# Kernel tuning notes

Hardware: AMD Instinct MI355X
Metric: run time of the kernel (lower is better)

Reference implementation:

```python
import jax, jax.numpy as jnp
import numpy as np

HID = 128          # args.hidden_dim
B = 8              # batch_size
N = 256            # num_nodes per graph (uniform)
L = 48             # num_colours / levels per graph (uniform, logk=False)
CELLS = B * N * L  # 98304 'cell' nodes
E = 250000         # edges per edge type
STEPS = 2          # args.msg_passing_steps


def setup_inputs() -> dict:
    key = jax.random.key(0)
    ks = jax.random.split(key, 20)
    s = 0.05
    d = {}
    d["q"] = jax.random.randint(ks[0], (CELLS,), 0, 3)
    d["edge_src"] = jax.random.randint(ks[1], (2, E), 0, CELLS)
    d["edge_dst"] = jax.random.randint(ks[2], (2, E), 0, CELLS)
    d["embed"] = jax.random.normal(ks[3], (3, HID), jnp.float32) * s
    # per-edge-type 4-layer MLP (stacked along axis 0: [intra, inter])
    d["msg_W0"] = jax.random.normal(ks[4], (2, HID, 2 * HID), jnp.float32) * s
    d["msg_b0"] = jnp.zeros((2, HID), jnp.float32)
    d["msg_W1"] = jax.random.normal(ks[5], (2, HID, HID), jnp.float32) * s
    d["msg_b1"] = jnp.zeros((2, HID), jnp.float32)
    d["msg_W2"] = jax.random.normal(ks[6], (2, HID, HID), jnp.float32) * s
    d["msg_b2"] = jnp.zeros((2, HID), jnp.float32)
    d["msg_W3"] = jax.random.normal(ks[7], (2, HID, HID), jnp.float32) * s
    d["msg_b3"] = jnp.zeros((2, HID), jnp.float32)
    # LSTMCell, bias=False: input = cat(x, m_intra, m_inter) -> 3*HID
    d["lstm_Wih"] = jax.random.normal(ks[8], (4 * HID, 3 * HID), jnp.float32) * s
    d["lstm_Whh"] = jax.random.normal(ks[9], (4 * HID, HID), jnp.float32) * s
    d["score_w"] = jax.random.normal(ks[10], (1, HID), jnp.float32) * s
    return d


def reference(q, edge_src, edge_dst, embed, msg_W0, msg_b0, msg_W1, msg_b1,
              msg_W2, msg_b2, msg_W3, msg_b3, lstm_Wih, lstm_Whh, score_w):
    x = embed[q]  # [CELLS, HID]

    def edge_msgs(h):
        msgs = []
        for et in range(2):  # structural loop over the 2 edge types
            src, dst = edge_src[et], edge_dst[et]
            m = jnp.concatenate([h[src], h[dst]], axis=-1)  # [E, 2H]
            m = jax.nn.relu(m @ msg_W0[et].T + msg_b0[et])
            m = jax.nn.relu(m @ msg_W1[et].T + msg_b1[et])
            m = jax.nn.relu(m @ msg_W2[et].T + msg_b2[et])
            m = m @ msg_W3[et].T + msg_b3[et]
            msgs.append(jax.ops.segment_sum(m, dst, num_segments=CELLS))
        return msgs

    def step(carry, _):
        h, rh, rc = carry
        m_intra, m_inter = edge_msgs(h)
        lstm_in = jnp.concatenate([x, m_intra, m_inter], axis=-1)  # [CELLS, 3H]
        gates = lstm_in @ lstm_Wih.T + rh @ lstm_Whh.T              # [CELLS, 4H]
        i, f, g, o = jnp.split(gates, 4, axis=-1)
        nc = jax.nn.sigmoid(f) * rc + jax.nn.sigmoid(i) * jnp.tanh(g)
        nh = jax.nn.sigmoid(o) * jnp.tanh(nc)
        return (nh, nh, nc), nh

    zeros = jnp.zeros_like(x)
    _, outs = jax.lax.scan(step, (x, zeros, zeros), None, length=STEPS)
    # outs: [STEPS, CELLS, HID]; uniform sizes make get_padded_tensor a reshape:
    # [STEPS, B, L, N, HID] -> score -> view(STEPS, B*N*L)
    logits = (outs @ score_w[0]).reshape(STEPS, B * L * N)
    return logits
```

## Files before the change

### kernel.cpp

```cpp
#include <hip/hip_runtime.h>

#define HID 128
#define CELLS 98304
#define NE 250000
#define NSTEPS 2
#define NWIN 3912

typedef __attribute__((ext_vector_type(8))) short short8;
typedef __attribute__((ext_vector_type(4))) float f32x4;
typedef __attribute__((ext_vector_type(4))) unsigned int u32x4;
typedef unsigned short u16;

__device__ __forceinline__ int permf(int s) { return ((s & 7) << 4) | (s >> 3); }
__device__ __forceinline__ int nat_of_pos(int p) {
  int l = p & 63, hf = p >> 6;
  int slot = ((l >> 2) << 3) + (hf << 2) + (l & 3);
  return ((slot & 7) << 4) | (slot >> 3);
}

__device__ __forceinline__ u16 f2bf(float f) {
  unsigned int u = __builtin_bit_cast(unsigned int, f);
  u += 0x7fffu + ((u >> 16) & 1u);
  return (u16)(u >> 16);
}
__device__ __forceinline__ float bf2f(u16 s) {
  unsigned int u = ((unsigned int)s) << 16;
  return __builtin_bit_cast(float, u);
}
__device__ __forceinline__ unsigned int cvtpk_bf16(float lo, float hi) {
  unsigned int r;
  asm("v_cvt_pk_bf16_f32 %0, %1, %2" : "=v"(r) : "v"(lo), "v"(hi));
  return r;
}
__device__ __forceinline__ float sigm(float x) { return 1.f / (1.f + __expf(-x)); }
__device__ __forceinline__ float tanha(float x) { return 1.f - 2.f / (__expf(2.f * x) + 1.f); }

__device__ __forceinline__ void gload_lds16(const u16* g, u16* l) {
  __builtin_amdgcn_global_load_lds(
      (const __attribute__((address_space(1))) unsigned int*)(const void*)g,
      (__attribute__((address_space(3))) unsigned int*)(void*)l, 16, 0, 0);
}

__device__ __forceinline__ void stage_w(const u16* __restrict__ ws, u16* wl, int w, int lane) {
  #pragma unroll
  for (int i = 0; i < 2; ++i)
    gload_lds16(ws + i * 4096 + w * 512 + lane * 8, wl + i * 4096 + w * 512);
}

__global__ void prep_kernel(
    const float* __restrict__ W0, const float* __restrict__ W1,
    const float* __restrict__ W2, const float* __restrict__ W3,
    const float* __restrict__ b0, const float* __restrict__ b1,
    const float* __restrict__ b2, const float* __restrict__ b3,
    const float* __restrict__ Wih, const float* __restrict__ Whh,
    const float* __restrict__ embed, const float* __restrict__ sw,
    u16* __restrict__ W0b, u16* __restrict__ W123b,
    u16* __restrict__ Wcb, float* __restrict__ bp,
    u16* __restrict__ embp, float* __restrict__ swp)
{
  int idx = blockIdx.x * 256 + threadIdx.x;
  if (idx < 65536) {
    int et = idx >> 15, t = (idx >> 13) & 3, n = (idx >> 6) & 127, s = idx & 63;
    int g = s >> 3, j = s & 7;
    int gn = g ^ (n & 7);
    W0b[idx] = f2bf(W0[(et * 128 + n) * 256 + t * 64 + gn * 8 + j]);
    return;
  }
  idx -= 65536;
  if (idx < 98304) {
    int which = idx >> 15, r = idx & 32767;
    int et = r >> 14, hh = (r >> 13) & 1, n = (r >> 6) & 127, s = r & 63;
    int g = s >> 3, j = s & 7;
    int gn = g ^ (n & 7);
    const float* W = which == 0 ? W1 : (which == 1 ? W2 : W3);
    W123b[which * 32768 + r] = f2bf(W[(et * 128 + n) * 128 + permf(hh * 64 + gn * 8 + j)]);
    return;
  }
  idx -= 98304;
  if (idx < 262144) {
    int kc = idx >> 15, r = idx & 32767;
    int n = r >> 6, s = r & 63;
    int gp = s >> 3, j = s & 7;
    int k = kc * 64 + ((gp ^ (n & 7)) << 3) + j;
    int blk = k >> 7, s7 = k & 127;
    int k7 = (blk == 1 || blk == 2) ? nat_of_pos(s7) : s7;
    float v = (blk < 3) ? Wih[n * 384 + blk * 128 + k7] : Whh[n * 128 + k7];
    Wcb[idx] = f2bf(v);
    return;
  }
  idx -= 262144;
  if (idx < 1024) {
    int l = idx >> 8, r = idx & 255;
    int et = r >> 7, s = r & 127;
    const float* b = l == 0 ? b0 : (l == 1 ? b1 : (l == 2 ? b2 : b3));
    bp[idx] = b[et * 128 + permf(s)];
    return;
  }
  idx -= 1024;
  if (idx < 384) {
    embp[idx] = f2bf(embed[idx]);
    return;
  }
  idx -= 384;
  if (idx < 128) swp[idx] = sw[idx];
}

__global__ void init_kernel(const int* __restrict__ q, const u16* __restrict__ embp,
                            u16* __restrict__ xb, u16* __restrict__ h)
{
  int idx = blockIdx.x * 256 + threadIdx.x;
  int c = idx >> 7, s = idx & 127;
  u16 v = embp[q[c] * 128 + s];
  xb[idx] = v;
  h[idx] = v;
}

__global__ void hist_kernel(const int* __restrict__ edst, int* __restrict__ counts)
{
  int idx = blockIdx.x * 256 + threadIdx.x;
  if (idx >= 2 * NE) return;
  int et = (idx >= NE) ? 1 : 0;
  atomicAdd(&counts[et * CELLS + edst[idx]], 1);
}

__global__ void scan1_kernel(const int* __restrict__ counts, int* __restrict__ S,
                             int* __restrict__ btot)
{
  __shared__ int sh[1024];
  const int t = threadIdx.x, b = blockIdx.x;
  const int i = b * 1024 + t;
  int v = counts[i];
  sh[t] = v;
  __syncthreads();
  int acc = v;
  for (int off = 1; off < 1024; off <<= 1) {
    int add = (t >= off) ? sh[t - off] : 0;
    __syncthreads();
    acc += add;
    sh[t] = acc;
    __syncthreads();
  }
  S[i] = acc - v;
  if (t == 1023) btot[b] = acc;
}

__global__ void scan2_kernel(const int* __restrict__ btot, int* __restrict__ boffs,
                             int* __restrict__ S)
{
  __shared__ int sh[256];
  const int t = threadIdx.x;
  int v = (t < 192) ? btot[t] : 0;
  sh[t] = v;
  __syncthreads();
  int acc = v;
  for (int off = 1; off < 256; off <<= 1) {
    int add = (t >= off) ? sh[t - off] : 0;
    __syncthreads();
    acc += add;
    sh[t] = acc;
    __syncthreads();
  }
  if (t < 192) boffs[t] = acc - v;
  if (t == 0) S[2 * CELLS] = 2 * NE;
}

__global__ void scan3_kernel(int* __restrict__ S, const int* __restrict__ boffs)
{
  const int i = blockIdx.x * 1024 + threadIdx.x;
  S[i] += boffs[blockIdx.x];
}

__global__ void scatter_kernel(const int* __restrict__ esrc, const int* __restrict__ edst,
                               const int* __restrict__ S, int* __restrict__ fill,
                               int* __restrict__ ssrc, int* __restrict__ sdst)
{
  int idx = blockIdx.x * 256 + threadIdx.x;
  if (idx >= 2 * NE) return;
  int et = (idx >= NE) ? 1 : 0;
  int d = edst[idx];
  int pos = atomicAdd(&fill[et * CELLS + d], 1);
  int slot = S[et * CELLS + d] - et * NE + pos;
  sdst[et * NE + slot] = d;
  ssrc[et * NE + slot] = esrc[idx];
}

__device__ __forceinline__ void bias_relu_store(f32x4 (&acc)[4][8], const float* __restrict__ bl,
                                                u16* __restrict__ ab, int q, int c)
{
  float bias[8];
  #pragma unroll
  for (int j = 0; j < 8; ++j) bias[j] = bl[c * 8 + j];
  #pragma unroll
  for (int mt = 0; mt < 4; ++mt) {
    #pragma unroll
    for (int r = 0; r < 4; ++r) {
      const int rowl = mt * 16 + 4 * q + r;
      u32x4 t;
      #pragma unroll
      for (int p = 0; p < 4; ++p) {
        float v0 = acc[mt][2 * p][r] + bias[2 * p];
        float v1 = acc[mt][2 * p + 1][r] + bias[2 * p + 1];
        v0 = v0 > 0.f ? v0 : 0.f;
        v1 = v1 > 0.f ? v1 : 0.f;
        t[p] = cvtpk_bf16(v0, v1);
      }
      *(u32x4*)(ab + rowl * 128 + ((c ^ (rowl & 15)) << 3)) = t;
    }
  }
}

__launch_bounds__(512, 2)
__global__ void msg_kernel(
    const u16* __restrict__ h,
    const int* __restrict__ ssrc, const int* __restrict__ sdst,
    const int* __restrict__ S,
    const u16* __restrict__ W0b, const u16* __restrict__ W123b,
    const float* __restrict__ bp,
    u16* __restrict__ m0, u16* __restrict__ m1,
    int* __restrict__ side_dst, float* __restrict__ side_part)
{
  __shared__ u16 abuf[8][64 * 128];
  __shared__ u16 wbuf[2][128 * 64];
  const int et = blockIdx.y;
  const int tid = threadIdx.x;
  const int w = tid >> 6, lane = tid & 63, q = lane >> 4, c = lane & 15;
  const int ebase = blockIdx.x * 512 + w * 64;
  const int win = blockIdx.x * 8 + w;
  const int* __restrict__ src = ssrc + et * NE;
  const int* __restrict__ dst = sdst + et * NE;
  u16* __restrict__ msgs = (et == 0) ? m0 : m1;
  u16* ab = abuf[w];

  int eS = ebase + lane;
  if (eS >= NE) eS = NE - 1;
  const int srow = src[eS];

  int rowD[4];
  #pragma unroll
  for (int mt = 0; mt < 4; ++mt) {
    int e = ebase + mt * 16 + c;
    if (e >= NE) e = NE - 1;
    rowD[mt] = dst[e];
  }

  #pragma unroll
  for (int i = 0; i < 16; ++i) {
    const int r = i * 4 + (lane >> 4);
    const int grow = __shfl(srow, r);
    const int cg = lane & 15;
    gload_lds16(h + (size_t)grow * 128 + ((cg ^ (r & 15)) << 3), ab + i * 512);
  }
  stage_w(W0b + (et * 4 + 2) * 8192, wbuf[0], w, lane);

  const int eL = ebase + lane;
  const int dval = (eL < NE) ? dst[eL] : -1;
  int rpS = 0, rpE = 0;
  if (dval >= 0) {
    rpS = S[et * CELLS + dval] - et * NE;
    rpE = S[et * CELLS + dval + 1] - et * NE;
  }
  const int dlagged = __shfl_up(dval, 1);
  const bool headp = (lane == 0) | (dval != dlagged);
  const unsigned long long tails = (__ballot(headp) >> 1) | (1ull << 63);
  const unsigned long long intmask = __ballot(dval >= 0 && rpS >= ebase && rpE <= ebase + 64);

  const f32x4 zf = {0.f, 0.f, 0.f, 0.f};
  f32x4 acc[4][8];
  #pragma unroll
  for (int mt = 0; mt < 4; ++mt)
    #pragma unroll
    for (int nt = 0; nt < 8; ++nt) acc[mt][nt] = zf;

  asm volatile("s_waitcnt vmcnt(0)" ::: "memory");
  __syncthreads();

  #pragma unroll 1
  for (int i = 0; i < 10; ++i) {
    if (i < 9) {
      const int j = i + 1;
      const u16* wsrc;
      if (j < 4) {
        const int t = (j < 2) ? (j + 2) : (j - 2);
        wsrc = W0b + (et * 4 + t) * 8192;
      } else {
        const int li = j - 4;
        wsrc = W123b + (li >> 1) * 32768 + et * 16384 + (li & 1) * 8192;
      }
      stage_w(wsrc, wbuf[j & 1], w, lane);
    }
    if (i >= 4 && !(i & 1)) {
      bias_relu_store(acc, bp + ((i - 4) >> 1) * 256 + et * 128, ab, q, c);
      #pragma unroll
      for (int mt = 0; mt < 4; ++mt)
        #pragma unroll
        for (int nt = 0; nt < 8; ++nt) acc[mt][nt] = zf;
    }
    const u16* wb = wbuf[i & 1];
    #pragma unroll
    for (int ks = 0; ks < 2; ++ks) {
      short8 a[4], b[8];
      if (i < 2) {
        const int kqh = i * 64 + ks * 32 + q * 8;
        #pragma unroll
        for (int mt = 0; mt < 4; ++mt)
          a[mt] = *(const short8*)(h + (size_t)rowD[mt] * HID + kqh);
      } else {
        const int blk = (i & 1) * 8 + ks * 4 + q;
        #pragma unroll
        for (int mt = 0; mt < 4; ++mt) {
          const int row = mt * 16 + c;
          a[mt] = *(const short8*)(ab + row * 128 + ((blk ^ c) << 3));
        }
      }
      #pragma unroll
      for (int nt = 0; nt < 8; ++nt)
        b[nt] = *(const short8*)(wb + (nt * 16 + c) * 64 + (((ks * 4 + q) ^ (c & 7)) << 3));
      #pragma unroll
      for (int mt = 0; mt < 4; ++mt)
        #pragma unroll
        for (int nt = 0; nt < 8; ++nt)
          acc[mt][nt] = __builtin_amdgcn_mfma_f32_16x16x32_bf16(a[mt], b[nt], acc[mt][nt], 0, 0, 0);
    }
    asm volatile("s_waitcnt vmcnt(0)" ::: "memory");
    __syncthreads();
  }

  float bias[8];
  #pragma unroll
  for (int j = 0; j < 8; ++j) bias[j] = bp[3 * 256 + et * 128 + c * 8 + j];

  float* fab = (float*)ab;
  #pragma unroll
  for (int half = 0; half < 2; ++half) {
    #pragma unroll
    for (int mt = 0; mt < 4; ++mt) {
      #pragma unroll
      for (int r = 0; r < 4; ++r) {
        const int row = mt * 16 + 4 * q + r;
        f32x4 t;
        #pragma unroll
        for (int nti = 0; nti < 4; ++nti)
          t[nti] = acc[mt][half * 4 + nti][r] + bias[half * 4 + nti];
        *(f32x4*)(fab + row * 64 + c * 4) = t;
      }
    }
    float run = 0.f;
    int jstart = 0;
    #pragma unroll 1
    for (int jb = 0; jb < 64; jb += 8) {
      #pragma unroll
      for (int u = 0; u < 8; ++u) {
        const int j = jb + u;
        run += fab[j * 64 + lane];
        if ((tails >> j) & 1) {
          const int d = __builtin_amdgcn_readlane(dval, j);
          if (d >= 0) {
            if ((intmask >> j) & 1) {
              msgs[(size_t)d * HID + half * 64 + lane] = f2bf(run);
            } else {
              const int slot = (jstart == 0) ? 0 : 1;
              const size_t sb = ((size_t)et * NWIN + win) * 2 + slot;
              side_part[sb * 128 + half * 64 + lane] = run;
              if (lane == 0 && half == 0) side_dst[sb] = d;
            }
          }
          run = 0.f;
          jstart = j + 1;
        }
      }
    }
  }
}

__global__ void fixup_kernel(const int* __restrict__ S,
                             const int* __restrict__ side_dst,
                             const float* __restrict__ side_part,
                             u16* __restrict__ m0, u16* __restrict__ m1)
{
  const int b = blockIdx.x;
  const int et = b / NWIN, win = b - et * NWIN;
  const int t = threadIdx.x;
  u16* __restrict__ m = et ? m1 : m0;
  #pragma unroll
  for (int s = 0; s < 2; ++s) {
    const int d = side_dst[b * 2 + s];
    if (d < 0) continue;
    const int r0 = S[et * CELLS + d] - et * NE;
    if ((r0 >> 6) != win) continue;
    const int w1 = (S[et * CELLS + d + 1] - et * NE - 1) >> 6;
    float sum = 0.f;
    for (int wi = win; wi <= w1; ++wi) {
      const int base = (et * NWIN + wi) * 2;
      if (side_dst[base + 0] == d) sum += side_part[(size_t)(base + 0) * 128 + t];
      if (side_dst[base + 1] == d) sum += side_part[(size_t)(base + 1) * 128 + t];
    }
    m[(size_t)d * HID + t] = f2bf(sum);
  }
}

__launch_bounds__(512, 2)
__global__ void lstm_kernel(
    const int step,
    const u16* __restrict__ xb, const u16* __restrict__ mm0, const u16* __restrict__ mm1,
    u16* __restrict__ h, u16* __restrict__ rc,
    const u16* __restrict__ Wcb, const float* __restrict__ swp,
    const u16* __restrict__ zrow,
    float* __restrict__ out)
{
  __shared__ u16 wbuf[2][512 * 64];
  __shared__ u16 abuf[2][128 * 64];
  const int tid = threadIdx.x;
  const int cb = blockIdx.x * 128;
  const int w = tid >> 6, lane = tid & 63, q = lane >> 4, c = lane & 15;

  const f32x4 zf = {0.f, 0.f, 0.f, 0.f};
  f32x4 acc[8][4];
  #pragma unroll
  for (int mt = 0; mt < 8; ++mt)
    #pragma unroll
    for (int g = 0; g < 4; ++g) acc[mt][g] = zf;

  #define STAGE_A(kc, buf)                                                           \
    {                                                                                \
      _Pragma("unroll")                                                              \
      for (int i = 0; i < 2; ++i) {                                                  \
        const int idx = i * 512 + tid;                                               \
        const int cl = idx >> 3, lg = idx & 7;                                       \
        const int col = (((kc) & 1) << 6) + ((lg ^ (cl & 7)) << 3);                  \
        const int sel = (kc) >> 1;                                                   \
        const u16* srcp;                                                             \
        if (sel == 0)      srcp = xb  + (size_t)(cb + cl) * 128 + col;               \
        else if (sel == 1) srcp = mm0 + (size_t)(cb + cl) * 128 + col;               \
        else if (sel == 2) srcp = mm1 + (size_t)(cb + cl) * 128 + col;               \
        else srcp = (step == 0) ? (zrow + col) : (h + (size_t)(cb + cl) * 128 + col);\
        gload_lds16(srcp, abuf[buf] + i * 4096 + w * 512);                           \
      }                                                                              \
    }
  #define STAGE_W(kc, buf)                                                           \
    {                                                                                \
      _Pragma("unroll")                                                              \
      for (int i = 0; i < 8; ++i)                                                    \
        gload_lds16(Wcb + (size_t)(kc) * 32768 + i * 4096 + tid * 8,                 \
                    wbuf[buf] + i * 4096 + w * 512);                                 \
    }

  STAGE_A(0, 0);
  STAGE_W(0, 0);
  asm volatile("s_waitcnt vmcnt(0)" ::: "memory");
  __syncthreads();

  #pragma unroll 1
  for (int kc = 0; kc < 8; ++kc) {
    if (kc < 7) {
      STAGE_A(kc + 1, (kc + 1) & 1);
      STAGE_W(kc + 1, (kc + 1) & 1);
    }
    const u16* ac = abuf[kc & 1];
    const u16* wc = wbuf[kc & 1];
    #pragma unroll
    for (int kk = 0; kk < 2; ++kk) {
      const int lg = kk * 4 + q;
      short8 a[8], b[4];
      #pragma unroll
      for (int mt = 0; mt < 8; ++mt) {
        const int row = mt * 16 + c;
        a[mt] = *(const short8*)(ac + row * 64 + ((lg ^ (row & 7)) << 3));
      }
      #pragma unroll
      for (int g = 0; g < 4; ++g) {
        const int n = g * 128 + w * 16 + c;
        b[g] = *(const short8*)(wc + n * 64 + ((lg ^ (n & 7)) << 3));
      }
      #pragma unroll
      for (int mt = 0; mt < 8; ++mt)
        #pragma unroll
        for (int g = 0; g < 4; ++g)
          acc[mt][g] = __builtin_amdgcn_mfma_f32_16x16x32_bf16(a[mt], b[g], acc[mt][g], 0, 0, 0);
    }
    asm volatile("s_waitcnt vmcnt(0)" ::: "memory");
    __syncthreads();
  }
  #undef STAGE_A
  #undef STAGE_W

  const float swc = swp[w * 16 + c];
  const bool last = (step == NSTEPS - 1);
  float* pt = (float*)abuf;
  #pragma unroll
  for (int mt = 0; mt < 8; ++mt) {
    #pragma unroll
    for (int r = 0; r < 4; ++r) {
      const int cl = mt * 16 + 4 * q + r;
      const int cell = cb + cl;
      const float ig = sigm(acc[mt][0][r]);
      const float fg = sigm(acc[mt][1][r]);
      const float gg = tanha(acc[mt][2][r]);
      const float og = sigm(acc[mt][3][r]);
      u16* rcp = rc + (size_t)cell * HID + w * 16 + c;
      const float c0 = (step == 0) ? 0.f : bf2f(rcp[0]);
      const float nc = fg * c0 + ig * gg;
      const float nhv = og * tanha(nc);
      if (!last) {
        rcp[0] = f2bf(nc);
        h[(size_t)cell * HID + w * 16 + c] = f2bf(nhv);
      }
      float v = nhv * swc;
      v += __shfl_xor(v, 1); v += __shfl_xor(v, 2);
      v += __shfl_xor(v, 4); v += __shfl_xor(v, 8);
      if (c == 0) pt[w * 128 + cl] = v;
    }
  }
  __syncthreads();
  if (tid < 128) {
    float s = 0.f;
    #pragma unroll
    for (int ww = 0; ww < 8; ++ww) s += pt[ww * 128 + tid];
    out[step * CELLS + cb + tid] = s;
  }
}

extern "C" void kernel_launch(void* const* d_in, const int* in_sizes, int n_in,
                              void* d_out, int out_size, void* d_ws, size_t ws_size,
                              hipStream_t stream)
{
  const int* q      = (const int*)d_in[0];
  const int* esrc   = (const int*)d_in[1];
  const int* edst   = (const int*)d_in[2];
  const float* embed= (const float*)d_in[3];
  const float* W0   = (const float*)d_in[4];
  const float* b0   = (const float*)d_in[5];
  const float* W1   = (const float*)d_in[6];
  const float* b1   = (const float*)d_in[7];
  const float* W2   = (const float*)d_in[8];
  const float* b2   = (const float*)d_in[9];
  const float* W3   = (const float*)d_in[10];
  const float* b3   = (const float*)d_in[11];
  const float* Wih  = (const float*)d_in[12];
  const float* Whh  = (const float*)d_in[13];
  const float* sw   = (const float*)d_in[14];

  char* ws = (char*)d_ws;
  size_t off = 0;
  auto alloc = [&](size_t bytes) {
    void* p = ws + off;
    off += (bytes + 255) & ~(size_t)255;
    return p;
  };
  u16*   h    = (u16*)  alloc((size_t)CELLS * HID * 2);
  u16*   xb   = (u16*)  alloc((size_t)CELLS * HID * 2);
  u16*   rc   = (u16*)  alloc((size_t)CELLS * HID * 2);
  u16*   m0   = (u16*)  alloc((size_t)CELLS * HID * 2);
  u16*   m1   = (u16*)  alloc((size_t)CELLS * HID * 2);
  u16*   W0b  = (u16*)  alloc(2 * 128 * 256 * 2);
  u16*   W123b= (u16*)  alloc((size_t)3 * 2 * 128 * 128 * 2);
  u16*   Wcb  = (u16*)  alloc(512 * 512 * 2);
  float* bp   = (float*)alloc(4 * 256 * 4);
  u16*   embp = (u16*)  alloc(384 * 2);
  float* swp  = (float*)alloc(128 * 4);
  u16*   zrow = (u16*)  alloc(128 * 2);
  int*   counts = (int*)alloc((size_t)2 * CELLS * 4);
  int*   Sarr   = (int*)alloc(((size_t)2 * CELLS + 1) * 4);
  int*   fill   = (int*)alloc((size_t)2 * CELLS * 4);
  int*   btot   = (int*)alloc(192 * 4);
  int*   boffs  = (int*)alloc(192 * 4);
  int*   ssrc   = (int*)alloc((size_t)2 * NE * 4);
  int*   sdst   = (int*)alloc((size_t)2 * NE * 4);
  int*   side_dst  = (int*)  alloc((size_t)2 * NWIN * 2 * 4);
  float* side_part = (float*)alloc((size_t)2 * NWIN * 2 * 128 * 4);

  prep_kernel<<<1670, 256, 0, stream>>>(W0, W1, W2, W3, b0, b1, b2, b3, Wih, Whh, embed, sw,
                                        W0b, W123b, Wcb, bp, embp, swp);
  init_kernel<<<(CELLS * HID) / 256, 256, 0, stream>>>(q, embp, xb, h);

  hipMemsetAsync(counts, 0, (size_t)2 * CELLS * 4, stream);
  hipMemsetAsync(fill, 0, (size_t)2 * CELLS * 4, stream);
  hist_kernel<<<(2 * NE + 255) / 256, 256, 0, stream>>>(edst, counts);
  scan1_kernel<<<192, 1024, 0, stream>>>(counts, Sarr, btot);
  scan2_kernel<<<1, 256, 0, stream>>>(btot, boffs, Sarr);
  scan3_kernel<<<192, 1024, 0, stream>>>(Sarr, boffs);
  scatter_kernel<<<(2 * NE + 255) / 256, 256, 0, stream>>>(esrc, edst, Sarr, fill, ssrc, sdst);

  hipMemsetAsync(m0, 0, (size_t)2 * CELLS * HID * 2, stream);
  hipMemsetAsync(side_dst, 0xFF, (size_t)2 * NWIN * 2 * 4, stream);
  hipMemsetAsync(zrow, 0, 128 * 2, stream);

  for (int step = 0; step < NSTEPS; ++step) {
    msg_kernel<<<dim3((NE + 511) / 512, 2), 512, 0, stream>>>(h, ssrc, sdst, Sarr,
                                                              W0b, W123b, bp,
                                                              m0, m1, side_dst, side_part);
    fixup_kernel<<<2 * NWIN, 128, 0, stream>>>(Sarr, side_dst, side_part, m0, m1);
    lstm_kernel<<<CELLS / 128, 512, 0, stream>>>(step, xb, m0, m1, h, rc, Wcb, swp, zrow,
                                                 (float*)d_out);
  }
}
```

Baseline: 674.2 us.

## Load LSTM activations directly from global and give each wave private weight buffers

The LSTM gate GEMM stops staging the activation tile through shared memory. Each wave now reads its A fragments straight from global memory and double-buffers only its own slice of the weight matrix in a per-wave LDS region, so the block-wide barriers inside the K loop go away. It also skips the recurrent-hidden K chunks on step 0, where h is zero, which drops the zero-row buffer. The cost is uncoalesced, redundant global reads of activations: all eight waves now load the same A rows.

```diff
diff --git a/kernel.cpp b/kernel.cpp
--- a/kernel.cpp
+++ b/kernel.cpp
@@ -404,11 +404,10 @@
     const u16* __restrict__ xb, const u16* __restrict__ mm0, const u16* __restrict__ mm1,
     u16* __restrict__ h, u16* __restrict__ rc,
     const u16* __restrict__ Wcb, const float* __restrict__ swp,
-    const u16* __restrict__ zrow,
     float* __restrict__ out)
 {
-  __shared__ u16 wbuf[2][512 * 64];
-  __shared__ u16 abuf[2][128 * 64];
+  __shared__ u16 wbuf[8][2][4096];
+  __shared__ float pshare[8 * 128];
   const int tid = threadIdx.x;
   const int cb = blockIdx.x * 128;
   const int w = tid >> 6, lane = tid & 63, q = lane >> 4, c = lane & 15;
@@ -420,57 +419,37 @@
     #pragma unroll
     for (int g = 0; g < 4; ++g) acc[mt][g] = zf;
 
-  #define STAGE_A(kc, buf)                                                           \
-    {                                                                                \
-      _Pragma("unroll")                                                              \
-      for (int i = 0; i < 2; ++i) {                                                  \
-        const int idx = i * 512 + tid;                                               \
-        const int cl = idx >> 3, lg = idx & 7;                                       \
-        const int col = (((kc) & 1) << 6) + ((lg ^ (cl & 7)) << 3);                  \
-        const int sel = (kc) >> 1;                                                   \
-        const u16* srcp;                                                             \
-        if (sel == 0)      srcp = xb  + (size_t)(cb + cl) * 128 + col;               \
-        else if (sel == 1) srcp = mm0 + (size_t)(cb + cl) * 128 + col;               \
-        else if (sel == 2) srcp = mm1 + (size_t)(cb + cl) * 128 + col;               \
-        else srcp = (step == 0) ? (zrow + col) : (h + (size_t)(cb + cl) * 128 + col);\
-        gload_lds16(srcp, abuf[buf] + i * 4096 + w * 512);                           \
-      }                                                                              \
-    }
-  #define STAGE_W(kc, buf)                                                           \
-    {                                                                                \
-      _Pragma("unroll")                                                              \
-      for (int i = 0; i < 8; ++i)                                                    \
-        gload_lds16(Wcb + (size_t)(kc) * 32768 + i * 4096 + tid * 8,                 \
-                    wbuf[buf] + i * 4096 + w * 512);                                 \
-    }
-
-  STAGE_A(0, 0);
+  #define STAGE_W(kc, buf)                                                     \
+    { _Pragma("unroll")                                                        \
+      for (int g = 0; g < 4; ++g)                                              \
+        _Pragma("unroll")                                                      \
+        for (int i = 0; i < 2; ++i)                                            \
+          gload_lds16(Wcb + (size_t)(kc) * 32768 + (g * 128 + w * 16) * 64     \
+                          + i * 512 + lane * 8,                                \
+                      &wbuf[w][buf][g * 1024 + i * 512]);                      \
+    }
+
   STAGE_W(0, 0);
   asm volatile("s_waitcnt vmcnt(0)" ::: "memory");
-  __syncthreads();
-
+
+  const int kmax = (step == 0) ? 6 : 8;
   #pragma unroll 1
-  for (int kc = 0; kc < 8; ++kc) {
-    if (kc < 7) {
-      STAGE_A(kc + 1, (kc + 1) & 1);
-      STAGE_W(kc + 1, (kc + 1) & 1);
-    }
-    const u16* ac = abuf[kc & 1];
-    const u16* wc = wbuf[kc & 1];
+  for (int kc = 0; kc < kmax; ++kc) {
+    const int sel = kc >> 1;
+    const u16* ab2 = (sel == 0) ? xb : (sel == 1) ? mm0 : (sel == 2) ? mm1 : h;
+    const int colb = (kc & 1) * 64;
+    const u16* wc = wbuf[w][kc & 1];
     #pragma unroll
     for (int kk = 0; kk < 2; ++kk) {
       const int lg = kk * 4 + q;
       short8 a[8], b[4];
       #pragma unroll
-      for (int mt = 0; mt < 8; ++mt) {
-        const int row = mt * 16 + c;
-        a[mt] = *(const short8*)(ac + row * 64 + ((lg ^ (row & 7)) << 3));
-      }
-      #pragma unroll
-      for (int g = 0; g < 4; ++g) {
-        const int n = g * 128 + w * 16 + c;
-        b[g] = *(const short8*)(wc + n * 64 + ((lg ^ (n & 7)) << 3));
-      }
+      for (int mt = 0; mt < 8; ++mt)
+        a[mt] = *(const short8*)(ab2 + (size_t)(cb + mt * 16 + c) * 128 + colb + lg * 8);
+      if (kk == 0 && kc + 1 < kmax) STAGE_W(kc + 1, (kc + 1) & 1);
+      #pragma unroll
+      for (int g = 0; g < 4; ++g)
+        b[g] = *(const short8*)(wc + g * 1024 + c * 64 + ((lg ^ (c & 7)) << 3));
       #pragma unroll
       for (int mt = 0; mt < 8; ++mt)
         #pragma unroll
@@ -478,14 +457,11 @@
           acc[mt][g] = __builtin_amdgcn_mfma_f32_16x16x32_bf16(a[mt], b[g], acc[mt][g], 0, 0, 0);
     }
     asm volatile("s_waitcnt vmcnt(0)" ::: "memory");
-    __syncthreads();
-  }
-  #undef STAGE_A
+  }
   #undef STAGE_W
 
   const float swc = swp[w * 16 + c];
   const bool last = (step == NSTEPS - 1);
-  float* pt = (float*)abuf;
   #pragma unroll
   for (int mt = 0; mt < 8; ++mt) {
     #pragma unroll
@@ -507,14 +483,14 @@
       float v = nhv * swc;
       v += __shfl_xor(v, 1); v += __shfl_xor(v, 2);
       v += __shfl_xor(v, 4); v += __shfl_xor(v, 8);
-      if (c == 0) pt[w * 128 + cl] = v;
+      if (c == 0) pshare[w * 128 + cl] = v;
     }
   }
   __syncthreads();
   if (tid < 128) {
     float s = 0.f;
     #pragma unroll
-    for (int ww = 0; ww < 8; ++ww) s += pt[ww * 128 + tid];
+    for (int ww = 0; ww < 8; ++ww) s += pshare[ww * 128 + tid];
     out[step * CELLS + cb + tid] = s;
   }
 }
@@ -557,7 +533,6 @@
   float* bp   = (float*)alloc(4 * 256 * 4);
   u16*   embp = (u16*)  alloc(384 * 2);
   float* swp  = (float*)alloc(128 * 4);
-  u16*   zrow = (u16*)  alloc(128 * 2);
   int*   counts = (int*)alloc((size_t)2 * CELLS * 4);
   int*   Sarr   = (int*)alloc(((size_t)2 * CELLS + 1) * 4);
   int*   fill   = (int*)alloc((size_t)2 * CELLS * 4);
@@ -582,14 +557,13 @@
 
   hipMemsetAsync(m0, 0, (size_t)2 * CELLS * HID * 2, stream);
   hipMemsetAsync(side_dst, 0xFF, (size_t)2 * NWIN * 2 * 4, stream);
-  hipMemsetAsync(zrow, 0, 128 * 2, stream);
 
   for (int step = 0; step < NSTEPS; ++step) {
     msg_kernel<<<dim3((NE + 511) / 512, 2), 512, 0, stream>>>(h, ssrc, sdst, Sarr,
                                                               W0b, W123b, bp,
                                                               m0, m1, side_dst, side_part);
     fixup_kernel<<<2 * NWIN, 128, 0, stream>>>(Sarr, side_dst, side_part, m0, m1);
-    lstm_kernel<<<CELLS / 128, 512, 0, stream>>>(step, xb, m0, m1, h, rc, Wcb, swp, zrow,
+    lstm_kernel<<<CELLS / 128, 512, 0, stream>>>(step, xb, m0, m1, h, rc, Wcb, swp,
                                                  (float*)d_out);
   }
 }
```

After: 742.3 us. 10.1% more time.
